# Performance work log

Measured on AMD Instinct MI355X. Metric: run time of the kernel, lower is better.

## Reference

```python
import jax, jax.numpy as jnp
import numpy as np

D = 1024
H = 16
HD = D // H
EPS = 1e-5


def layer_norm(x, g, b):
    mu = jnp.mean(x, axis=-1, keepdims=True)
    var = jnp.var(x, axis=-1, keepdims=True)
    return (x - mu) * jax.lax.rsqrt(var + EPS) * g + b


def setup_inputs() -> dict:
    key = jax.random.key(0)
    ks = jax.random.split(key, 16)
    s = 0.02
    return {
        "x": jax.random.normal(ks[0], (2, 2048, D), jnp.float32),
        "ln1_g": jnp.ones((D,), jnp.float32),
        "ln1_b": jnp.zeros((D,), jnp.float32),
        "Wq": jax.random.normal(ks[1], (D, D), jnp.float32) * s,
        "bq": jnp.zeros((D,), jnp.float32),
        "Wk": jax.random.normal(ks[2], (D, D), jnp.float32) * s,
        "bk": jnp.zeros((D,), jnp.float32),
        "Wv": jax.random.normal(ks[3], (D, D), jnp.float32) * s,
        "bv": jnp.zeros((D,), jnp.float32),
        "Wo": jax.random.normal(ks[4], (D, D), jnp.float32) * s,
        "bo": jnp.zeros((D,), jnp.float32),
        "ln2_g": jnp.ones((D,), jnp.float32),
        "ln2_b": jnp.zeros((D,), jnp.float32),
        "W1": jax.random.normal(ks[5], (D, 4 * D), jnp.float32) * s,
        "b1": jnp.zeros((4 * D,), jnp.float32),
        "W2": jax.random.normal(ks[6], (4 * D, D), jnp.float32) * s,
        "b2": jnp.zeros((D,), jnp.float32),
    }


def reference(x, ln1_g, ln1_b, Wq, bq, Wk, bk, Wv, bv, Wo, bo, ln2_g, ln2_b, W1, b1, W2, b2):
    B, T, _ = x.shape
    # --- attention sub-block (pre-LN) ---
    h = layer_norm(x, ln1_g, ln1_b)
    q = (h @ Wq + bq).reshape(B, T, H, HD).transpose(0, 2, 1, 3)  # [B,H,T,hd]
    k = (h @ Wk + bk).reshape(B, T, H, HD).transpose(0, 2, 1, 3)
    v = (h @ Wv + bv).reshape(B, T, H, HD).transpose(0, 2, 1, 3)
    scores = jnp.einsum("bhqd,bhkd->bhqk", q, k)  # full O(T^2) scores as in source
    causal = jnp.tril(jnp.ones((T, T), bool))
    scores = jnp.where(causal, scores, -jnp.inf)
    w = jax.nn.softmax(scores / np.sqrt(HD), axis=-1)
    ctx = jnp.einsum("bhqk,bhkd->bhqd", w, v)
    ctx = ctx.transpose(0, 2, 1, 3).reshape(B, T, D)
    x = x + (ctx @ Wo + bo)
    # --- MLP sub-block (pre-LN) ---
    h = layer_norm(x, ln2_g, ln2_b)
    h = jax.nn.gelu(h @ W1 + b1, approximate=False)
    x = x + (h @ W2 + b2)
    return x
```

## Files before the change

kernel.cpp:

```cpp
#include <hip/hip_runtime.h>
#include <math.h>


typedef _Float16 half8 __attribute__((ext_vector_type(8)));
typedef _Float16 half4v __attribute__((ext_vector_type(4)));
typedef float floatx4 __attribute__((ext_vector_type(4)));

#define DMODEL 1024
#define SEQT   2048
#define NTOK   4096
#define NHEAD  16
#define HDIM   64

__device__ __forceinline__ void llds16(const _Float16* g, _Float16* l) {
  __builtin_amdgcn_global_load_lds(
      (const __attribute__((address_space(1))) void*)g,
      (__attribute__((address_space(3))) void*)l, 16, 0, 0);
}

__global__ __launch_bounds__(256) void prep_kernel(
    const float* __restrict__ x, const float* __restrict__ g,
    const float* __restrict__ b, _Float16* __restrict__ h16out,
    const float* __restrict__ Wq, const float* __restrict__ Wk,
    const float* __restrict__ Wv, const float* __restrict__ Wo,
    const float* __restrict__ W1, const float* __restrict__ W2,
    _Float16* __restrict__ wt_base) {
  const int t256 = threadIdx.x;
  if (blockIdx.x < 4096) {
    int row = blockIdx.x;
    const float4 xv = ((const float4*)(x + (size_t)row * DMODEL))[t256];
    float s = xv.x + xv.y + xv.z + xv.w;
    float s2 = xv.x * xv.x + xv.y * xv.y + xv.z * xv.z + xv.w * xv.w;
#pragma unroll
    for (int off = 32; off; off >>= 1) {
      s += __shfl_down(s, off);
      s2 += __shfl_down(s2, off);
    }
    __shared__ float red[8];
    int wid = t256 >> 6;
    if ((t256 & 63) == 0) { red[wid] = s; red[wid + 4] = s2; }
    __syncthreads();
    s = red[0] + red[1] + red[2] + red[3];
    s2 = red[4] + red[5] + red[6] + red[7];
    float mu = s * (1.0f / DMODEL);
    float var = s2 * (1.0f / DMODEL) - mu * mu;
    float rstd = rsqrtf(var + 1e-5f);
    const float4 gv = ((const float4*)g)[t256];
    const float4 bv = ((const float4*)b)[t256];
    half4v o;
    o[0] = (_Float16)((xv.x - mu) * rstd * gv.x + bv.x);
    o[1] = (_Float16)((xv.y - mu) * rstd * gv.y + bv.y);
    o[2] = (_Float16)((xv.z - mu) * rstd * gv.z + bv.z);
    o[3] = (_Float16)((xv.w - mu) * rstd * gv.w + bv.w);
    *(half4v*)(h16out + (size_t)row * DMODEL + t256 * 4) = o;
    return;
  }
  __shared__ float lb[64][65];
  int id = blockIdx.x - 4096;
  const float* src; _Float16* dst; int K, N, t;
  if (id < 1024) {
    int s = id >> 8;
    src = (s == 0) ? Wq : (s == 1) ? Wk : (s == 2) ? Wv : Wo;
    dst = wt_base + (size_t)s * (1024 * 1024);
    K = 1024; N = 1024; t = id & 255;
  } else if (id < 2048) {
    src = W1; dst = wt_base + (size_t)4 * 1024 * 1024; K = 1024; N = 4096; t = id - 1024;
  } else {
    src = W2; dst = wt_base + (size_t)8 * 1024 * 1024; K = 4096; N = 1024; t = id - 2048;
  }
  int tilesN = N >> 6;
  int tk = t / tilesN, tn = t % tilesN;
#pragma unroll
  for (int i = 0; i < 4; ++i) {
    int row = i * 16 + (t256 >> 4);
    int c4 = (t256 & 15) * 4;
    float4 v = *(const float4*)&src[(size_t)(tk * 64 + row) * N + tn * 64 + c4];
    lb[row][c4] = v.x; lb[row][c4 + 1] = v.y;
    lb[row][c4 + 2] = v.z; lb[row][c4 + 3] = v.w;
  }
  __syncthreads();
  {
    int r = t256 >> 2, cb = t256 & 3;
    half8 h0, h1;
#pragma unroll
    for (int kk = 0; kk < 8; ++kk) h0[kk] = (_Float16)lb[cb * 16 + kk][r];
#pragma unroll
    for (int kk = 0; kk < 8; ++kk) h1[kk] = (_Float16)lb[cb * 16 + 8 + kk][r];
    _Float16* dp = dst + (size_t)(tn * 64 + r) * K + tk * 64 + cb * 16;
    *(half8*)dp = h0;
    *(half8*)(dp + 8) = h1;
  }
}

__global__ __launch_bounds__(256) void ln_kernel(
    const float* __restrict__ x, const float* __restrict__ g,
    const float* __restrict__ b, _Float16* __restrict__ out) {
  int row = blockIdx.x;
  int t = threadIdx.x;
  const float4 xv = ((const float4*)(x + (size_t)row * DMODEL))[t];
  float s = xv.x + xv.y + xv.z + xv.w;
  float s2 = xv.x * xv.x + xv.y * xv.y + xv.z * xv.z + xv.w * xv.w;
#pragma unroll
  for (int off = 32; off; off >>= 1) {
    s += __shfl_down(s, off);
    s2 += __shfl_down(s2, off);
  }
  __shared__ float red[8];
  int wid = t >> 6;
  if ((t & 63) == 0) { red[wid] = s; red[wid + 4] = s2; }
  __syncthreads();
  s = red[0] + red[1] + red[2] + red[3];
  s2 = red[4] + red[5] + red[6] + red[7];
  float mu = s * (1.0f / DMODEL);
  float var = s2 * (1.0f / DMODEL) - mu * mu;
  float rstd = rsqrtf(var + 1e-5f);
  const float4 gv = ((const float4*)g)[t];
  const float4 bv = ((const float4*)b)[t];
  half4v o;
  o[0] = (_Float16)((xv.x - mu) * rstd * gv.x + bv.x);
  o[1] = (_Float16)((xv.y - mu) * rstd * gv.y + bv.y);
  o[2] = (_Float16)((xv.z - mu) * rstd * gv.z + bv.z);
  o[3] = (_Float16)((xv.w - mu) * rstd * gv.w + bv.w);
  *(half4v*)(out + (size_t)row * DMODEL + t * 4) = o;
}

template <int OUTMODE>
__global__ __launch_bounds__(256) void gemmw_kernel(
    const _Float16* __restrict__ A, const _Float16* __restrict__ Bt0, int K,
    const float* __restrict__ bias0, const float* __restrict__ bias1,
    const float* __restrict__ bias2, const float* __restrict__ res,
    float* __restrict__ outf, _Float16* __restrict__ outh) {
  __shared__ __align__(16) _Float16 As[2][128 * 64];
  __shared__ __align__(16) _Float16 Bs[2][64 * 64];
  const int tid = threadIdx.x;
  const int m0 = blockIdx.x * 128;
  const int w = tid >> 6, lane = tid & 63;
  const int l15 = lane & 15, q8 = lane >> 4;
  const int wrow = w * 32;
  const _Float16* Bt;
  const float* bias;
  _Float16* outh_sel = outh;
  int n0, sel = 0;
  if (OUTMODE == 2) {
    sel = blockIdx.y >> 4;
    n0 = (blockIdx.y & 15) * 64;
    Bt = Bt0 + (size_t)sel * (1024 * 1024);
    bias = (sel == 0) ? bias0 : (sel == 1) ? bias1 : bias2;
    outh_sel = outh + (size_t)sel * ((size_t)NTOK * DMODEL);
  } else {
    n0 = blockIdx.y * 64;
    Bt = Bt0;
    bias = bias0;
  }

  const _Float16* gA[4]; int la[4];
  const _Float16* gB[2]; int lb2[2];
#pragma unroll
  for (int i = 0; i < 4; ++i) {
    int c = i * 256 + tid;
    int r = c >> 3, gc = ((c & 7) ^ (r & 7)) * 8;
    gA[i] = A + (size_t)(m0 + r) * K + gc;
    la[i] = c * 8;
  }
#pragma unroll
  for (int i = 0; i < 2; ++i) {
    int c = i * 256 + tid;
    int r = c >> 3, gc = ((c & 7) ^ (r & 7)) * 8;
    gB[i] = Bt + (size_t)(n0 + r) * K + gc;
    lb2[i] = c * 8;
  }
  auto stage = [&](int buf) {
#pragma unroll
    for (int i = 0; i < 4; ++i) {
      llds16(gA[i], &As[buf][la[i]]);
      gA[i] += 64;
    }
#pragma unroll
    for (int i = 0; i < 2; ++i) {
      llds16(gB[i], &Bs[buf][lb2[i]]);
      gB[i] += 64;
    }
  };

  floatx4 acc[2][4];
#pragma unroll
  for (int i = 0; i < 2; ++i)
#pragma unroll
    for (int j = 0; j < 4; ++j) acc[i][j] = (floatx4){0.f, 0.f, 0.f, 0.f};

  const int nk = K >> 6;
  stage(0);
  __syncthreads();
  for (int t = 0; t < nk; ++t) {
    const int buf = t & 1;
    if (t + 1 < nk) stage(buf ^ 1);
    half8 af[2][2], bf[4][2];
#pragma unroll
    for (int i = 0; i < 2; ++i) {
      int rA = wrow + i * 16 + l15;
#pragma unroll
      for (int kh = 0; kh < 2; ++kh) {
        int sl = ((kh * 4 + q8) ^ (rA & 7)) * 8;
        af[i][kh] = *(const half8*)&As[buf][rA * 64 + sl];
      }
    }
#pragma unroll
    for (int j = 0; j < 4; ++j) {
      int rB = j * 16 + l15;
#pragma unroll
      for (int kh = 0; kh < 2; ++kh) {
        int sl = ((kh * 4 + q8) ^ (rB & 7)) * 8;
        bf[j][kh] = *(const half8*)&Bs[buf][rB * 64 + sl];
      }
    }
#pragma unroll
    for (int i = 0; i < 2; ++i)
#pragma unroll
      for (int j = 0; j < 4; ++j) {
        acc[i][j] = __builtin_amdgcn_mfma_f32_16x16x32_f16(af[i][0], bf[j][0], acc[i][j], 0, 0, 0);
        acc[i][j] = __builtin_amdgcn_mfma_f32_16x16x32_f16(af[i][1], bf[j][1], acc[i][j], 0, 0, 0);
      }
    __syncthreads();
  }

#pragma unroll
  for (int i = 0; i < 2; ++i) {
    int rowb = m0 + wrow + i * 16 + q8 * 4;
#pragma unroll
    for (int j = 0; j < 4; ++j) {
      int col = n0 + j * 16 + l15;
      float bval = bias[col];
      if (OUTMODE == 2 && sel == 2) {
        int bb = rowb >> 11, tt0 = rowb & 2047;
        int hh = col >> 6, hd = col & 63;
        half4v hv;
#pragma unroll
        for (int r = 0; r < 4; ++r) hv[r] = (_Float16)(acc[i][j][r] + bval);
        *(half4v*)&outh_sel[((size_t)(bb * NHEAD + hh) * HDIM + hd) * SEQT + tt0] = hv;
      } else {
#pragma unroll
        for (int r = 0; r < 4; ++r) {
          int row = rowb + r;
          float v = acc[i][j][r] + bval;
          if (OUTMODE == 0) {
            v += res[(size_t)row * 1024 + col];
            outf[(size_t)row * 1024 + col] = v;
          } else if (OUTMODE == 1) {
            float z = 1.5957691216f * v * (1.0f + 0.044715f * v * v);
            float gl = v / (1.0f + __expf(-z));
            outh[(size_t)row * 4096 + col] = (_Float16)gl;
          } else {
            int bb = row >> 11, tt = row & 2047;
            int hh = col >> 6, hd = col & 63;
            outh_sel[((size_t)(bb * NHEAD + hh) * SEQT + tt) * HDIM + hd] = (_Float16)v;
          }
        }
      }
    }
  }
}

__global__ __launch_bounds__(256) void attn_kernel(
    const _Float16* __restrict__ q, const _Float16* __restrict__ k,
    const _Float16* __restrict__ vt, _Float16* __restrict__ ctx) {
  __shared__ __align__(16) _Float16 Ks[2][64 * 64];
  __shared__ __align__(16) _Float16 Vs[2][64 * 64];
  __shared__ __align__(16) _Float16 Ps[64 * 72];
  __shared__ float Lpart[4][64];
  const int tid = threadIdx.x;
  const int w = tid >> 6, lane = tid & 63;
  const int l15 = lane & 15, q8 = lane >> 4;
  const int bh = blockIdx.y;
  const int pr = blockIdx.x;
  const size_t base = (size_t)bh * SEQT * HDIM;

  const _Float16* gk0[2]; const _Float16* gv0[2]; int ldsc[2];
#pragma unroll
  for (int i = 0; i < 2; ++i) {
    int c = i * 256 + w * 64 + lane;
    int r = c >> 3, gc = ((c & 7) ^ (r & 7)) * 8;
    gk0[i] = k + base + (size_t)r * HDIM + gc;
    gv0[i] = vt + base + (size_t)r * SEQT + gc;
    ldsc[i] = c * 8;
  }
  auto stage = [&](int kt, int buf) {
#pragma unroll
    for (int i = 0; i < 2; ++i) {
      llds16(gk0[i] + (size_t)kt * (64 * HDIM), &Ks[buf][ldsc[i]]);
      llds16(gv0[i] + kt * 64, &Vs[buf][ldsc[i]]);
    }
  };

  const int rswA = (l15 & 7);
  const int cs0 = (q8 ^ rswA) * 8;
  const int cs1 = ((4 + q8) ^ rswA) * 8;

  int s = 0;
  stage(0, 0);
  __syncthreads();
  for (int ph = 0; ph < 2; ++ph) {
    const int qtile = ph ? 31 - pr : pr;
    const int ntile = qtile + 1;
    half8 bq[4][2];
#pragma unroll
    for (int nt = 0; nt < 4; ++nt) {
      const half8* qp = (const half8*)(q + base + (size_t)(qtile * 64 + nt * 16 + l15) * HDIM);
      bq[nt][0] = qp[q8];
      bq[nt][1] = qp[4 + q8];
    }
    floatx4 acc[4];
#pragma unroll
    for (int j = 0; j < 4; ++j) acc[j] = (floatx4){0.f, 0.f, 0.f, 0.f};
    float lsum[4] = {0.f, 0.f, 0.f, 0.f};

    for (int jt = 0; jt < ntile; ++jt, ++s) {
      const int buf = s & 1;
      if (s + 1 < 33) {
        int sn = s + 1;
        int nkt = (sn <= pr) ? sn : sn - (pr + 1);
        stage(nkt, buf ^ 1);
      }
      half8 ak0 = *(const half8*)&Ks[buf][(w * 16 + l15) * 64 + cs0];
      half8 ak1 = *(const half8*)&Ks[buf][(w * 16 + l15) * 64 + cs1];
      floatx4 sv[4];
#pragma unroll
      for (int nt = 0; nt < 4; ++nt) {
        sv[nt] = __builtin_amdgcn_mfma_f32_16x16x32_f16(ak0, bq[nt][0],
                                                        (floatx4){0.f, 0.f, 0.f, 0.f}, 0, 0, 0);
        sv[nt] = __builtin_amdgcn_mfma_f32_16x16x32_f16(ak1, bq[nt][1], sv[nt], 0, 0, 0);
      }
      const bool diag = (jt == ntile - 1);
#pragma unroll
      for (int nt = 0; nt < 4; ++nt) {
        half4v phv;
#pragma unroll
        for (int r = 0; r < 4; ++r) {
          float p = __expf(sv[nt][r] * 0.125f);
          if (diag) {
            p = (w * 16 + q8 * 4 + r <= nt * 16 + l15) ? p : 0.f;
          }
          lsum[nt] += p;
          phv[r] = (_Float16)p;
        }
        *(half4v*)&Ps[(nt * 16 + l15) * 72 + w * 16 + q8 * 4] = phv;
      }
      asm volatile("s_waitcnt lgkmcnt(0)" ::: "memory");
      __builtin_amdgcn_s_barrier();
      asm volatile("" ::: "memory");
      half8 ap0 = *(const half8*)&Ps[(w * 16 + l15) * 72 + q8 * 8];
      half8 ap1 = *(const half8*)&Ps[(w * 16 + l15) * 72 + 32 + q8 * 8];
#pragma unroll
      for (int ntd = 0; ntd < 4; ++ntd) {
        half8 bv0 = *(const half8*)&Vs[buf][(ntd * 16 + l15) * 64 + cs0];
        half8 bv1 = *(const half8*)&Vs[buf][(ntd * 16 + l15) * 64 + cs1];
        acc[ntd] = __builtin_amdgcn_mfma_f32_16x16x32_f16(ap0, bv0, acc[ntd], 0, 0, 0);
        acc[ntd] = __builtin_amdgcn_mfma_f32_16x16x32_f16(ap1, bv1, acc[ntd], 0, 0, 0);
      }
      __syncthreads();
    }

#pragma unroll
    for (int nt = 0; nt < 4; ++nt) {
      lsum[nt] += __shfl_xor(lsum[nt], 16);
      lsum[nt] += __shfl_xor(lsum[nt], 32);
      if (q8 == 0) Lpart[w][nt * 16 + l15] = lsum[nt];
    }
    __syncthreads();
    const int b = bh >> 4, h = bh & 15;
#pragma unroll
    for (int r = 0; r < 4; ++r) {
      int qr = w * 16 + q8 * 4 + r;
      float inv = 1.0f / (Lpart[0][qr] + Lpart[1][qr] + Lpart[2][qr] + Lpart[3][qr]);
      int tg = qtile * 64 + qr;
      _Float16* op = ctx + ((size_t)(b * SEQT + tg)) * DMODEL + h * HDIM;
#pragma unroll
      for (int ntd = 0; ntd < 4; ++ntd)
        op[ntd * 16 + l15] = (_Float16)(acc[ntd][r] * inv);
    }
  }
}

extern "C" void kernel_launch(void* const* d_in, const int* in_sizes, int n_in,
                              void* d_out, int out_size, void* d_ws, size_t ws_size,
                              hipStream_t stream) {
  (void)in_sizes; (void)n_in; (void)out_size; (void)ws_size;
  const float* x    = (const float*)d_in[0];
  const float* ln1g = (const float*)d_in[1];
  const float* ln1b = (const float*)d_in[2];
  const float* Wq   = (const float*)d_in[3];
  const float* bq   = (const float*)d_in[4];
  const float* Wk   = (const float*)d_in[5];
  const float* bk   = (const float*)d_in[6];
  const float* Wv   = (const float*)d_in[7];
  const float* bv   = (const float*)d_in[8];
  const float* Wo   = (const float*)d_in[9];
  const float* bo   = (const float*)d_in[10];
  const float* ln2g = (const float*)d_in[11];
  const float* ln2b = (const float*)d_in[12];
  const float* W1   = (const float*)d_in[13];
  const float* b1   = (const float*)d_in[14];
  const float* W2   = (const float*)d_in[15];
  const float* b2   = (const float*)d_in[16];
  float* out = (float*)d_out;

  char* ws = (char*)d_ws;
  _Float16* wt    = (_Float16*)(ws);
  _Float16* h16   = (_Float16*)(ws + ((size_t)24 << 20));
  _Float16* qkv   = (_Float16*)(ws + ((size_t)32 << 20));
  _Float16* ctx16 = (_Float16*)(ws + ((size_t)24 << 20));
  float*    x1    = (float*)   (ws + ((size_t)32 << 20));
  _Float16* h2    = (_Float16*)(ws + ((size_t)48 << 20));
  _Float16* mid   = (_Float16*)(ws + ((size_t)56 << 20));

  const size_t QKV1 = (size_t)NTOK * DMODEL;

  prep_kernel<<<7168, 256, 0, stream>>>(x, ln1g, ln1b, h16,
                                        Wq, Wk, Wv, Wo, W1, W2, wt);
  gemmw_kernel<2><<<dim3(32, 48), 256, 0, stream>>>(
      h16, wt, 1024, bq, bk, bv, nullptr, nullptr, qkv);
  attn_kernel<<<dim3(16, 32), 256, 0, stream>>>(
      qkv, qkv + QKV1, qkv + 2 * QKV1, ctx16);
  gemmw_kernel<0><<<dim3(32, 16), 256, 0, stream>>>(
      ctx16, wt + (size_t)3 * 1024 * 1024, 1024, bo, nullptr, nullptr, x, x1, nullptr);
  ln_kernel<<<NTOK, 256, 0, stream>>>(x1, ln2g, ln2b, h2);
  gemmw_kernel<1><<<dim3(32, 64), 256, 0, stream>>>(
      h2, wt + (size_t)4 * 1024 * 1024, 1024, b1, nullptr, nullptr, nullptr,
      nullptr, mid);
  gemmw_kernel<0><<<dim3(32, 16), 256, 0, stream>>>(
      mid, wt + (size_t)8 * 1024 * 1024, 4096, b2, nullptr, nullptr, x1, out, nullptr);
}
```

Baseline: 338.3 us.

## Split-K the MLP down-projection GEMM into two halves with a reduction kernel

The final K=4096 GEMM is split into two K-halves across blockIdx.z, doubling the number of blocks to raise GPU occupancy. The first half writes bias plus residual plus its partial sum in fp32 to the output. The second half writes an fp16 partial into workspace (reusing the W1 weight region), and a new elementwise kernel adds it into the output. This adds a launch and an extra output-sized read/write pass, and rounds one partial sum to fp16.

```diff
diff --git a/kernel.cpp b/kernel.cpp
--- a/kernel.cpp
+++ b/kernel.cpp
@@ -122,6 +122,18 @@
   o[2] = (_Float16)((xv.z - mu) * rstd * gv.z + bv.z);
   o[3] = (_Float16)((xv.w - mu) * rstd * gv.w + bv.w);
   *(half4v*)(out + (size_t)row * DMODEL + t * 4) = o;
+}
+
+__global__ __launch_bounds__(256) void redux_kernel(
+    float* __restrict__ out, const _Float16* __restrict__ p1) {
+  size_t i = ((size_t)blockIdx.x * 256 + threadIdx.x) * 4;
+  float4 o = *(float4*)(out + i);
+  half4v a = *(const half4v*)(p1 + i);
+  o.x += (float)a[0];
+  o.y += (float)a[1];
+  o.z += (float)a[2];
+  o.w += (float)a[3];
+  *(float4*)(out + i) = o;
 }
 
 template <int OUTMODE>
@@ -152,6 +164,8 @@
     Bt = Bt0;
     bias = bias0;
   }
+  int Keff = K, koff = 0;
+  if (OUTMODE == 3) { Keff = K >> 1; koff = blockIdx.z * Keff; }
 
   const _Float16* gA[4]; int la[4];
   const _Float16* gB[2]; int lb2[2];
@@ -159,14 +173,14 @@
   for (int i = 0; i < 4; ++i) {
     int c = i * 256 + tid;
     int r = c >> 3, gc = ((c & 7) ^ (r & 7)) * 8;
-    gA[i] = A + (size_t)(m0 + r) * K + gc;
+    gA[i] = A + (size_t)(m0 + r) * K + koff + gc;
     la[i] = c * 8;
   }
 #pragma unroll
   for (int i = 0; i < 2; ++i) {
     int c = i * 256 + tid;
     int r = c >> 3, gc = ((c & 7) ^ (r & 7)) * 8;
-    gB[i] = Bt + (size_t)(n0 + r) * K + gc;
+    gB[i] = Bt + (size_t)(n0 + r) * K + koff + gc;
     lb2[i] = c * 8;
   }
   auto stage = [&](int buf) {
@@ -188,7 +202,7 @@
 #pragma unroll
     for (int j = 0; j < 4; ++j) acc[i][j] = (floatx4){0.f, 0.f, 0.f, 0.f};
 
-  const int nk = K >> 6;
+  const int nk = Keff >> 6;
   stage(0);
   __syncthreads();
   for (int t = 0; t < nk; ++t) {
@@ -241,18 +255,27 @@
 #pragma unroll
         for (int r = 0; r < 4; ++r) {
           int row = rowb + r;
-          float v = acc[i][j][r] + bval;
+          float v = acc[i][j][r];
           if (OUTMODE == 0) {
-            v += res[(size_t)row * 1024 + col];
+            v += bval + res[(size_t)row * 1024 + col];
             outf[(size_t)row * 1024 + col] = v;
           } else if (OUTMODE == 1) {
+            v += bval;
             float z = 1.5957691216f * v * (1.0f + 0.044715f * v * v);
             float gl = v / (1.0f + __expf(-z));
             outh[(size_t)row * 4096 + col] = (_Float16)gl;
-          } else {
+          } else if (OUTMODE == 2) {
+            v += bval;
             int bb = row >> 11, tt = row & 2047;
             int hh = col >> 6, hd = col & 63;
             outh_sel[((size_t)(bb * NHEAD + hh) * SEQT + tt) * HDIM + hd] = (_Float16)v;
+          } else {
+            if (blockIdx.z == 0) {
+              v += bval + res[(size_t)row * 1024 + col];
+              outf[(size_t)row * 1024 + col] = v;
+            } else {
+              outh[(size_t)row * 1024 + col] = (_Float16)v;
+            }
           }
         }
       }
@@ -411,6 +434,7 @@
   float*    x1    = (float*)   (ws + ((size_t)32 << 20));
   _Float16* h2    = (_Float16*)(ws + ((size_t)48 << 20));
   _Float16* mid   = (_Float16*)(ws + ((size_t)56 << 20));
+  _Float16* part1 = (_Float16*)(ws + ((size_t)8 << 20));
 
   const size_t QKV1 = (size_t)NTOK * DMODEL;
 
@@ -426,6 +450,7 @@
   gemmw_kernel<1><<<dim3(32, 64), 256, 0, stream>>>(
       h2, wt + (size_t)4 * 1024 * 1024, 1024, b1, nullptr, nullptr, nullptr,
       nullptr, mid);
-  gemmw_kernel<0><<<dim3(32, 16), 256, 0, stream>>>(
-      mid, wt + (size_t)8 * 1024 * 1024, 4096, b2, nullptr, nullptr, x1, out, nullptr);
-}
+  gemmw_kernel<3><<<dim3(32, 16, 2), 256, 0, stream>>>(
+      mid, wt + (size_t)8 * 1024 * 1024, 4096, b2, nullptr, nullptr, x1, out, part1);
+  redux_kernel<<<4096, 256, 0, stream>>>(out, part1);
+}
```

Result: slower. 345.2 us (+2.0%).
